# Kernel tuning notes

Hardware: AMD Instinct MI355X
Metric: run time of the kernel (lower is better)

## Reference

```python
import jax, jax.numpy as jnp
import numpy as np

DIM = 128; NH = 4; WH = 7; WW = 7
B = 16; H = 112; W = 112
SH, SW = WH // 2, WW // 2          # shift sizes (3,3)
NWIN = WH * WW                     # 49 tokens per window
HEAD = DIM // NH


def _rel_pos_index():
    ch, cw = np.meshgrid(np.arange(WH), np.arange(WW), indexing='ij')
    coords = np.stack([ch, cw]).reshape(2, -1)            # (2, NWIN)
    rel = coords[:, :, None] - coords[:, None, :]          # (2, NWIN, NWIN)
    rel = rel.transpose(1, 2, 0).copy()
    rel[:, :, 0] += WH - 1
    rel[:, :, 1] += WW - 1
    rel[:, :, 0] *= 2 * WW - 1
    return rel.sum(-1)                                     # (NWIN, NWIN) int


def _shift_mask():
    img = np.zeros((H, W), dtype=np.float32)
    cnt = 0
    for hs in (slice(0, -WH), slice(-WH, -SH), slice(-SH, None)):
        for ws in (slice(0, -WW), slice(-WW, -SW), slice(-SW, None)):
            img[hs, ws] = cnt
            cnt += 1
    mw = img.reshape(H // WH, WH, W // WW, WW).transpose(0, 2, 1, 3).reshape(-1, NWIN)
    diff = mw[:, None, :] - mw[:, :, None]                 # (nW, NWIN, NWIN)
    return np.where(diff != 0, -100.0, 0.0).astype(np.float32)


REL_IDX = jnp.asarray(_rel_pos_index())                    # (NWIN, NWIN) int32
MASK = jnp.asarray(_shift_mask())                          # (nW, NWIN, NWIN)


def setup_inputs() -> dict:
    key = jax.random.key(0)
    k = jax.random.split(key, 6)
    s = 0.02
    return {
        'x': jax.random.normal(k[0], (B, H, W, DIM), dtype=jnp.float32),
        'qkv_w': jax.random.normal(k[1], (3 * DIM, DIM), dtype=jnp.float32) * s,
        'qkv_b': jnp.zeros((3 * DIM,), dtype=jnp.float32),
        'proj_w': jax.random.normal(k[2], (DIM, DIM), dtype=jnp.float32) * s,
        'proj_b': jnp.zeros((DIM,), dtype=jnp.float32),
        'rpb_table': jax.random.normal(k[3], ((2 * WH - 1) * (2 * WW - 1), NH), dtype=jnp.float32) * s,
    }


def reference(x, qkv_w, qkv_b, proj_w, proj_b, rpb_table):
    scale = HEAD ** -0.5
    Bx, Hh, Ww, C = x.shape
    Nh, Nw = Hh // WH, Ww // WW
    nW = Nh * Nw
    # cyclic shift
    x = jnp.roll(x, shift=(-SH, -SW), axis=(1, 2))
    # window partition -> (B*nW, NWIN, C)
    xw = x.reshape(Bx, Nh, WH, Nw, WW, C).transpose(0, 1, 3, 2, 4, 5).reshape(-1, NWIN, C)
    # fused qkv projection, split (T, Nh, P) on last dim
    qkv = (xw @ qkv_w.T + qkv_b).reshape(-1, NWIN, 3, NH, HEAD).transpose(2, 0, 3, 1, 4)
    q, k, v = qkv[0] * scale, qkv[1], qkv[2]               # (Bn, NH, NWIN, HEAD)
    attn = jnp.einsum('bhid,bhjd->bhij', q, k)             # (Bn, NH, NWIN, NWIN)
    # relative position bias gather
    bias = rpb_table[REL_IDX.reshape(-1)].reshape(NWIN, NWIN, NH).transpose(2, 0, 1)
    attn = attn + bias[None]
    # shift mask (broadcast over batch and heads)
    attn = attn.reshape(Bx, nW, NH, NWIN, NWIN) + MASK[None, :, None]
    attn = jax.nn.softmax(attn, axis=-1).reshape(-1, NH, NWIN, NWIN)
    out = jnp.einsum('bhij,bhjd->bhid', attn, v)           # (Bn, NH, NWIN, HEAD)
    out = out.transpose(0, 2, 1, 3).reshape(-1, NWIN, C)   # head-major concat
    out = out @ proj_w.T + proj_b
    # window merge + reverse shift
    out = out.reshape(Bx, Nh, Nw, WH, WW, C).transpose(0, 1, 3, 2, 4, 5).reshape(Bx, Hh, Ww, C)
    out = jnp.roll(out, shift=(SH, SW), axis=(1, 2))
    return out
```

## Files before the change

kernel.cpp:

```cpp
#include <hip/hip_runtime.h>
#include <hip/hip_bf16.h>

typedef __attribute__((ext_vector_type(8))) short short8;
typedef __attribute__((ext_vector_type(4))) float floatx4;

#define IMGH 112
#define IMGW 112
#define SHIFT 3
#define NWIN 49

#define XSTR 152
#define QKSTR 280
#define VTSTR 88

#define LOG2E 1.4426950408889634f
#define QSCALE (0.17677669529663687f * LOG2E)
#define NMASK (-100.0f * LOG2E)

__device__ inline unsigned short f2bf1(float f) {
    unsigned r;
    asm("v_cvt_pk_bf16_f32 %0, %1, %1" : "=v"(r) : "v"(f));
    return (unsigned short)r;
}
__device__ inline unsigned cvtpk(float lo, float hi) {
    unsigned r;
    asm("v_cvt_pk_bf16_f32 %0, %1, %2" : "=v"(r) : "v"(lo), "v"(hi));
    return r;
}

__device__ inline floatx4 mfma16(short8 a, short8 b, floatx4 c) {
    return __builtin_amdgcn_mfma_f32_16x16x32_bf16(a, b, c, 0, 0, 0);
}
__device__ inline floatx4 zero4() {
    floatx4 z; z[0] = 0.f; z[1] = 0.f; z[2] = 0.f; z[3] = 0.f; return z;
}
__device__ inline short8 ones8() {
    short8 z;
    #pragma unroll
    for (int i = 0; i < 8; ++i) z[i] = (short)0x3F80;
    return z;
}

__global__ __launch_bounds__(256) void convert_w(const float* __restrict__ qkv_w,
                                                 const float* __restrict__ proj_w,
                                                 short* __restrict__ ws) {
    int i = blockIdx.x * 256 + threadIdx.x;
    if (i < 49152) {
        float v = qkv_w[i];
        if (i < 16384) v *= QSCALE;
        ws[i] = (short)f2bf1(v);
    }
    if (i < 16384) ws[49152 + i] = (short)f2bf1(proj_w[i]);
}

__global__ __launch_bounds__(512, 4) void win_attn_mfma8(
    const float* __restrict__ x,
    const float* __restrict__ qkv_b,
    const float* __restrict__ proj_b,
    const float* __restrict__ rpb,
    const short* __restrict__ wq,
    const short* __restrict__ wp,
    float* __restrict__ out)
{
    __shared__ alignas(16) short s_xp[64 * XSTR];
    __shared__ alignas(16) short s_qk[64 * QKSTR];
    __shared__ alignas(16) short s_vt[128 * VTSTR];
    __shared__ float2 s_rpb[2][169];
    __shared__ int s_meta[64];
    __shared__ int s_gout[64];

    const int tid = threadIdx.x;
    const int w    = tid >> 6;
    const int l    = tid & 63;
    const int l15  = l & 15;
    const int lg   = l >> 4;
    const int hgrp = w >> 2;
    const int m_w  = w & 3;

    const int blk = blockIdx.x;
    const int b   = blk >> 8;
    const int wi  = blk & 255;
    const int hs0 = (wi >> 4) * 7;
    const int ws0 = (wi & 15) * 7;

    const float* xb = x + (size_t)b * (IMGH * IMGW * 128);

    if (tid < 64) {
        int rowc = tid < NWIN ? tid : NWIN - 1;
        int ri = (rowc * 9363) >> 16;
        int ci = rowc - ri * 7;
        int hc = hs0 + ri, wc = ws0 + ci;
        int reg = (hc < 105 ? 0 : (hc < 109 ? 1 : 2)) * 3
                + (wc < 105 ? 0 : (wc < 109 ? 1 : 2));
        if (tid >= NWIN) reg = 255;
        s_meta[tid] = (ri * 13 + ci) | (reg << 8);
        int gh = hc + SHIFT; if (gh >= IMGH) gh -= IMGH;
        int gw = wc + SHIFT; if (gw >= IMGW) gw -= IMGW;
        s_gout[tid] = gh * IMGW + gw;
    }
    if (tid < 338) {
        int hg  = tid < 169 ? 0 : 1;
        int idx = tid - hg * 169;
        float2 v = *(const float2*)(rpb + idx * 4 + hg * 2);
        v.x *= LOG2E; v.y *= LOG2E;
        s_rpb[hg][idx] = v;
    }
    {
        int row  = tid >> 3;
        int col0 = (tid & 7) << 4;
        uint4 u0 = {0,0,0,0}, u1 = {0,0,0,0};
        if (row < NWIN) {
            int rr = (row * 9363) >> 16;
            int cc = row - rr * 7;
            int gh = hs0 + rr + SHIFT; if (gh >= IMGH) gh -= IMGH;
            int gw = ws0 + cc + SHIFT; if (gw >= IMGW) gw -= IMGW;
            const float* px = xb + (((size_t)(gh * IMGW + gw)) << 7) + col0;
            float4 a = *(const float4*)(px + 0);
            float4 c4 = *(const float4*)(px + 4);
            float4 e = *(const float4*)(px + 8);
            float4 g = *(const float4*)(px + 12);
            u0.x = cvtpk(a.x, a.y);   u0.y = cvtpk(a.z, a.w);
            u0.z = cvtpk(c4.x, c4.y); u0.w = cvtpk(c4.z, c4.w);
            u1.x = cvtpk(e.x, e.y);   u1.y = cvtpk(e.z, e.w);
            u1.z = cvtpk(g.x, g.y);   u1.w = cvtpk(g.z, g.w);
        }
        *(uint4*)&s_xp[row * XSTR + col0]     = u0;
        *(uint4*)&s_xp[row * XSTR + col0 + 8] = u1;
    }
    __syncthreads();

    {
        short8 bfr[3][4];
        float  biasr[3];
        #pragma unroll
        for (int i = 0; i < 3; ++i) {
            int j0 = (w * 3 + i) << 4;
            const short* wb = wq + ((j0 + l15) << 7) + lg * 8;
            #pragma unroll
            for (int kk = 0; kk < 4; ++kk) bfr[i][kk] = *(const short8*)(wb + kk * 32);
            float bb = qkv_b[j0 + l15];
            biasr[i] = (j0 < 128) ? bb * QSCALE : bb;
        }
        for (int m = 0; m < 4; ++m) {
            short8 af[4];
            #pragma unroll
            for (int kk = 0; kk < 4; ++kk)
                af[kk] = *(const short8*)&s_xp[(m * 16 + l15) * XSTR + kk * 32 + lg * 8];
            floatx4 acc[3];
            #pragma unroll
            for (int i = 0; i < 3; ++i) acc[i] = zero4();
            #pragma unroll
            for (int kk = 0; kk < 4; ++kk)
                #pragma unroll
                for (int i = 0; i < 3; ++i)
                    acc[i] = mfma16(af[kk], bfr[i][kk], acc[i]);
            #pragma unroll
            for (int i = 0; i < 3; ++i) {
                int j0 = (w * 3 + i) << 4;
                #pragma unroll
                for (int c = 0; c < 4; ++c) {
                    int row = m * 16 + lg * 4 + c;
                    unsigned short v = f2bf1(acc[i][c] + biasr[i]);
                    if (j0 < 256) s_qk[row * QKSTR + j0 + l15] = (short)v;
                    else          s_vt[(j0 - 256 + l15) * VTSTR + row] = (short)v;
                }
            }
        }
    }
    __syncthreads();

    float2 b2[4][4];
    {
        int mj[4];
        #pragma unroll
        for (int n = 0; n < 4; ++n) mj[n] = s_meta[n * 16 + l15];
        #pragma unroll
        for (int c = 0; c < 4; ++c) {
            int mi = s_meta[m_w * 16 + lg * 4 + c];
            int ti = mi & 255, gi = mi >> 8;
            #pragma unroll
            for (int n = 0; n < 4; ++n) {
                int d = ti - (mj[n] & 255) + 84;
                float msk = (gi == (mj[n] >> 8)) ? 0.f : NMASK;
                float2 r2 = s_rpb[hgrp][d];
                b2[c][n].x = r2.x + msk;
                b2[c][n].y = r2.y + msk;
            }
        }
    }

    floatx4 accO[2][2];
    float   inv[2][4];
    const short8 vone = ones8();
    #pragma unroll
    for (int hh = 0; hh < 2; ++hh) {
        const int h = hgrp * 2 + hh;
        short8 qf = *(const short8*)&s_qk[(m_w * 16 + l15) * QKSTR + h * 32 + lg * 8];
        floatx4 accS[4];
        #pragma unroll
        for (int n = 0; n < 4; ++n) {
            short8 kf = *(const short8*)&s_qk[(n * 16 + l15) * QKSTR + 128 + h * 32 + lg * 8];
            accS[n] = mfma16(qf, kf, zero4());
        }
        float p[4][4];
        #pragma unroll
        for (int n = 0; n < 4; ++n)
            #pragma unroll
            for (int c = 0; c < 4; ++c)
                p[n][c] = exp2f(accS[n][c] + (hh ? b2[c][n].y : b2[c][n].x));
        #pragma unroll
        for (int n = 0; n < 4; ++n)
            #pragma unroll
            for (int c = 0; c < 4; ++c)
                s_xp[(m_w * 16 + lg * 4 + c) * XSTR + hgrp * 72 + n * 16 + l15] =
                    (short)f2bf1(p[n][c]);
        short8 pa[2];
        #pragma unroll
        for (int kt = 0; kt < 2; ++kt)
            pa[kt] = *(const short8*)&s_xp[(m_w * 16 + l15) * XSTR + hgrp * 72 + kt * 32 + lg * 8];
        floatx4 accSum = zero4();
        #pragma unroll
        for (int vt = 0; vt < 2; ++vt) accO[hh][vt] = zero4();
        #pragma unroll
        for (int kt = 0; kt < 2; ++kt) {
            #pragma unroll
            for (int vt = 0; vt < 2; ++vt) {
                short8 vf = *(const short8*)&s_vt[(h * 32 + vt * 16 + l15) * VTSTR + kt * 32 + lg * 8];
                accO[hh][vt] = mfma16(pa[kt], vf, accO[hh][vt]);
            }
            accSum = mfma16(pa[kt], vone, accSum);
        }
        #pragma unroll
        for (int c = 0; c < 4; ++c) inv[hh][c] = 1.f / accSum[c];
    }
    __syncthreads();

    #pragma unroll
    for (int hh = 0; hh < 2; ++hh)
        #pragma unroll
        for (int vt = 0; vt < 2; ++vt)
            #pragma unroll
            for (int c = 0; c < 4; ++c)
                s_xp[(m_w * 16 + lg * 4 + c) * XSTR + hgrp * 64 + hh * 32 + vt * 16 + l15] =
                    (short)f2bf1(accO[hh][vt][c] * inv[hh][c]);
    __syncthreads();

    {
        floatx4 acc[4];
        #pragma unroll
        for (int m = 0; m < 4; ++m) acc[m] = zero4();
        const short* wbp = wp + ((w * 16 + l15) << 7) + lg * 8;
        #pragma unroll
        for (int kk = 0; kk < 4; ++kk) {
            short8 bfr = *(const short8*)(wbp + kk * 32);
            #pragma unroll
            for (int m = 0; m < 4; ++m) {
                short8 of = *(const short8*)&s_xp[(m * 16 + l15) * XSTR + kk * 32 + lg * 8];
                acc[m] = mfma16(of, bfr, acc[m]);
            }
        }
        float bias = proj_b[w * 16 + l15];
        const size_t obase = (size_t)b * (IMGH * IMGW);
        #pragma unroll
        for (int m = 0; m < 4; ++m)
            #pragma unroll
            for (int c = 0; c < 4; ++c) {
                int row = m * 16 + lg * 4 + c;
                if (row < NWIN)
                    out[((obase + s_gout[row]) << 7) + w * 16 + l15] = acc[m][c] + bias;
            }
    }
}

extern "C" void kernel_launch(void* const* d_in, const int* in_sizes, int n_in,
                              void* d_out, int out_size, void* d_ws, size_t ws_size,
                              hipStream_t stream) {
    const float* x      = (const float*)d_in[0];
    const float* qkv_w  = (const float*)d_in[1];
    const float* qkv_b  = (const float*)d_in[2];
    const float* proj_w = (const float*)d_in[3];
    const float* proj_b = (const float*)d_in[4];
    const float* rpb    = (const float*)d_in[5];
    float* out = (float*)d_out;
    short* wbf = (short*)d_ws;

    hipLaunchKernelGGL(convert_w, dim3(192), dim3(256), 0, stream, qkv_w, proj_w, wbf);
    hipLaunchKernelGGL(win_attn_mfma8, dim3(4096), dim3(512), 0, stream,
                       x, qkv_b, proj_b, rpb, wbf, wbf + 49152, out);
}
```

Measured before the change: 109.5 us.

## Swap MFMA operand order to produce transposed tiles enabling vectorized stores

Swaps the A/B operands of several MFMA calls (Q/K projection, QK^T, PV, row-sum, output projection) so each lane's four accumulator values lie along contiguous columns instead of rows. This lets the kernel pack results into uint2 bf16 stores to LDS and float4 stores to global output, replacing many scalar 2-byte and 4-byte writes. The bias and mask metadata loads are reorganized to match the transposed layout, and the softmax normalizer becomes one scalar per lane. The risk is that LDS bank conflicts or register pressure shift with the new access patterns.

```diff
diff --git a/kernel.cpp b/kernel.cpp
--- a/kernel.cpp
+++ b/kernel.cpp
@@ -131,66 +131,70 @@
 
     {
         short8 bfr[3][4];
-        float  biasr[3];
+        float4 biasq[3];
+        float  biasv[3];
         #pragma unroll
         for (int i = 0; i < 3; ++i) {
             int j0 = (w * 3 + i) << 4;
             const short* wb = wq + ((j0 + l15) << 7) + lg * 8;
             #pragma unroll
             for (int kk = 0; kk < 4; ++kk) bfr[i][kk] = *(const short8*)(wb + kk * 32);
-            float bb = qkv_b[j0 + l15];
-            biasr[i] = (j0 < 128) ? bb * QSCALE : bb;
+            float4 b4 = *(const float4*)(qkv_b + j0 + lg * 4);
+            if (j0 < 128) { b4.x *= QSCALE; b4.y *= QSCALE; b4.z *= QSCALE; b4.w *= QSCALE; }
+            biasq[i] = b4;
+            biasv[i] = qkv_b[j0 + l15];
         }
         for (int m = 0; m < 4; ++m) {
             short8 af[4];
             #pragma unroll
             for (int kk = 0; kk < 4; ++kk)
                 af[kk] = *(const short8*)&s_xp[(m * 16 + l15) * XSTR + kk * 32 + lg * 8];
-            floatx4 acc[3];
-            #pragma unroll
-            for (int i = 0; i < 3; ++i) acc[i] = zero4();
-            #pragma unroll
-            for (int kk = 0; kk < 4; ++kk)
-                #pragma unroll
-                for (int i = 0; i < 3; ++i)
-                    acc[i] = mfma16(af[kk], bfr[i][kk], acc[i]);
             #pragma unroll
             for (int i = 0; i < 3; ++i) {
                 int j0 = (w * 3 + i) << 4;
-                #pragma unroll
-                for (int c = 0; c < 4; ++c) {
-                    int row = m * 16 + lg * 4 + c;
-                    unsigned short v = f2bf1(acc[i][c] + biasr[i]);
-                    if (j0 < 256) s_qk[row * QKSTR + j0 + l15] = (short)v;
-                    else          s_vt[(j0 - 256 + l15) * VTSTR + row] = (short)v;
+                if (j0 < 256) {
+                    floatx4 acc = zero4();
+                    #pragma unroll
+                    for (int kk = 0; kk < 4; ++kk) acc = mfma16(bfr[i][kk], af[kk], acc);
+                    uint2 u;
+                    u.x = cvtpk(acc[0] + biasq[i].x, acc[1] + biasq[i].y);
+                    u.y = cvtpk(acc[2] + biasq[i].z, acc[3] + biasq[i].w);
+                    *(uint2*)&s_qk[(m * 16 + l15) * QKSTR + j0 + lg * 4] = u;
+                } else {
+                    floatx4 acc = zero4();
+                    #pragma unroll
+                    for (int kk = 0; kk < 4; ++kk) acc = mfma16(af[kk], bfr[i][kk], acc);
+                    uint2 u;
+                    u.x = cvtpk(acc[0] + biasv[i], acc[1] + biasv[i]);
+                    u.y = cvtpk(acc[2] + biasv[i], acc[3] + biasv[i]);
+                    *(uint2*)&s_vt[(j0 - 256 + l15) * VTSTR + m * 16 + lg * 4] = u;
                 }
             }
         }
     }
     __syncthreads();
 
-    float2 b2[4][4];
-    {
-        int mj[4];
-        #pragma unroll
-        for (int n = 0; n < 4; ++n) mj[n] = s_meta[n * 16 + l15];
-        #pragma unroll
-        for (int c = 0; c < 4; ++c) {
-            int mi = s_meta[m_w * 16 + lg * 4 + c];
-            int ti = mi & 255, gi = mi >> 8;
-            #pragma unroll
-            for (int n = 0; n < 4; ++n) {
-                int d = ti - (mj[n] & 255) + 84;
-                float msk = (gi == (mj[n] >> 8)) ? 0.f : NMASK;
+    float b2x[4][4], b2y[4][4];
+    {
+        int mi = s_meta[m_w * 16 + l15];
+        int ti = mi & 255, gi = mi >> 8;
+        #pragma unroll
+        for (int n = 0; n < 4; ++n) {
+            int4 mk = *(const int4*)&s_meta[n * 16 + lg * 4];
+            #pragma unroll
+            for (int c = 0; c < 4; ++c) {
+                int mv = (&mk.x)[c];
+                int d = ti - (mv & 255) + 84;
+                float msk = (gi == (mv >> 8)) ? 0.f : NMASK;
                 float2 r2 = s_rpb[hgrp][d];
-                b2[c][n].x = r2.x + msk;
-                b2[c][n].y = r2.y + msk;
+                b2x[n][c] = r2.x + msk;
+                b2y[n][c] = r2.y + msk;
             }
         }
     }
 
     floatx4 accO[2][2];
-    float   inv[2][4];
+    float   inv2[2];
     const short8 vone = ones8();
     #pragma unroll
     for (int hh = 0; hh < 2; ++hh) {
@@ -200,20 +204,19 @@
         #pragma unroll
         for (int n = 0; n < 4; ++n) {
             short8 kf = *(const short8*)&s_qk[(n * 16 + l15) * QKSTR + 128 + h * 32 + lg * 8];
-            accS[n] = mfma16(qf, kf, zero4());
-        }
-        float p[4][4];
-        #pragma unroll
-        for (int n = 0; n < 4; ++n)
-            #pragma unroll
-            for (int c = 0; c < 4; ++c)
-                p[n][c] = exp2f(accS[n][c] + (hh ? b2[c][n].y : b2[c][n].x));
-        #pragma unroll
-        for (int n = 0; n < 4; ++n)
-            #pragma unroll
-            for (int c = 0; c < 4; ++c)
-                s_xp[(m_w * 16 + lg * 4 + c) * XSTR + hgrp * 72 + n * 16 + l15] =
-                    (short)f2bf1(p[n][c]);
+            accS[n] = mfma16(kf, qf, zero4());
+        }
+        #pragma unroll
+        for (int n = 0; n < 4; ++n) {
+            float p0 = exp2f(accS[n][0] + (hh ? b2y[n][0] : b2x[n][0]));
+            float p1 = exp2f(accS[n][1] + (hh ? b2y[n][1] : b2x[n][1]));
+            float p2 = exp2f(accS[n][2] + (hh ? b2y[n][2] : b2x[n][2]));
+            float p3 = exp2f(accS[n][3] + (hh ? b2y[n][3] : b2x[n][3]));
+            uint2 u;
+            u.x = cvtpk(p0, p1);
+            u.y = cvtpk(p2, p3);
+            *(uint2*)&s_xp[(m_w * 16 + l15) * XSTR + hgrp * 72 + n * 16 + lg * 4] = u;
+        }
         short8 pa[2];
         #pragma unroll
         for (int kt = 0; kt < 2; ++kt)
@@ -226,23 +229,23 @@
             #pragma unroll
             for (int vt = 0; vt < 2; ++vt) {
                 short8 vf = *(const short8*)&s_vt[(h * 32 + vt * 16 + l15) * VTSTR + kt * 32 + lg * 8];
-                accO[hh][vt] = mfma16(pa[kt], vf, accO[hh][vt]);
-            }
-            accSum = mfma16(pa[kt], vone, accSum);
-        }
-        #pragma unroll
-        for (int c = 0; c < 4; ++c) inv[hh][c] = 1.f / accSum[c];
+                accO[hh][vt] = mfma16(vf, pa[kt], accO[hh][vt]);
+            }
+            accSum = mfma16(vone, pa[kt], accSum);
+        }
+        inv2[hh] = 1.f / accSum[0];
     }
     __syncthreads();
 
     #pragma unroll
     for (int hh = 0; hh < 2; ++hh)
         #pragma unroll
-        for (int vt = 0; vt < 2; ++vt)
-            #pragma unroll
-            for (int c = 0; c < 4; ++c)
-                s_xp[(m_w * 16 + lg * 4 + c) * XSTR + hgrp * 64 + hh * 32 + vt * 16 + l15] =
-                    (short)f2bf1(accO[hh][vt][c] * inv[hh][c]);
+        for (int vt = 0; vt < 2; ++vt) {
+            uint2 u;
+            u.x = cvtpk(accO[hh][vt][0] * inv2[hh], accO[hh][vt][1] * inv2[hh]);
+            u.y = cvtpk(accO[hh][vt][2] * inv2[hh], accO[hh][vt][3] * inv2[hh]);
+            *(uint2*)&s_xp[(m_w * 16 + l15) * XSTR + hgrp * 64 + hh * 32 + vt * 16 + lg * 4] = u;
+        }
     __syncthreads();
 
     {
@@ -252,23 +255,27 @@
         const short* wbp = wp + ((w * 16 + l15) << 7) + lg * 8;
         #pragma unroll
         for (int kk = 0; kk < 4; ++kk) {
-            short8 bfr = *(const short8*)(wbp + kk * 32);
+            short8 pw = *(const short8*)(wbp + kk * 32);
             #pragma unroll
             for (int m = 0; m < 4; ++m) {
                 short8 of = *(const short8*)&s_xp[(m * 16 + l15) * XSTR + kk * 32 + lg * 8];
-                acc[m] = mfma16(of, bfr, acc[m]);
-            }
-        }
-        float bias = proj_b[w * 16 + l15];
+                acc[m] = mfma16(pw, of, acc[m]);
+            }
+        }
+        float4 pb = *(const float4*)(proj_b + w * 16 + lg * 4);
         const size_t obase = (size_t)b * (IMGH * IMGW);
         #pragma unroll
-        for (int m = 0; m < 4; ++m)
-            #pragma unroll
-            for (int c = 0; c < 4; ++c) {
-                int row = m * 16 + lg * 4 + c;
-                if (row < NWIN)
-                    out[((obase + s_gout[row]) << 7) + w * 16 + l15] = acc[m][c] + bias;
-            }
+        for (int m = 0; m < 4; ++m) {
+            int token = m * 16 + l15;
+            if (token < NWIN) {
+                float4 o4;
+                o4.x = acc[m][0] + pb.x;
+                o4.y = acc[m][1] + pb.y;
+                o4.z = acc[m][2] + pb.z;
+                o4.w = acc[m][3] + pb.w;
+                *(float4*)&out[((obase + s_gout[token]) << 7) + w * 16 + lg * 4] = o4;
+            }
+        }
     }
 }
 
```

Result: slower. 113.8 us (+3.8%).
